# Performance work log

Measured on AMD Instinct MI355X. Metric: run time of the kernel, lower is better.

Reference implementation:

```python
import jax, jax.numpy as jnp
import numpy as np

N, E, D, H, O, G = 50000, 640000, 128, 128, 16, 64


def setup_inputs() -> dict:
    key = jax.random.key(0)
    ks = jax.random.split(key, 10)
    x = jax.random.normal(ks[0], (N, D), dtype=jnp.float32)
    edge_index = jax.random.randint(ks[1], (2, E), 0, N, dtype=jnp.int64)
    edge_weight = jax.random.uniform(ks[2], (E,), dtype=jnp.float32)
    batch = jnp.sort(jax.random.randint(ks[3], (N,), 0, G, dtype=jnp.int64))
    s1 = 1.0 / np.sqrt(D)
    s2 = 1.0 / np.sqrt(H)
    W1 = jax.random.uniform(ks[4], (D, H), jnp.float32, -s1, s1)
    b1 = jnp.zeros((H,), jnp.float32)
    W2 = jax.random.uniform(ks[5], (H, H), jnp.float32, -s2, s2)
    b2 = jnp.zeros((H,), jnp.float32)
    Wfc = jax.random.uniform(ks[6], (H, O), jnp.float32, -s2, s2)
    bfc = jax.random.uniform(ks[7], (O,), jnp.float32, -s2, s2)
    return dict(x=x, edge_index=edge_index, edge_weight=edge_weight, batch=batch,
                W1=W1, b1=b1, W2=W2, b2=b2, Wfc=Wfc, bfc=bfc)


def _gcn_conv(x, row, col, ew, W, b, n):
    # PyG GCNConv: out[i] = sum_{(j->i)} norm_ji * (x[j] @ W) + b
    xw = x @ W
    deg = jax.ops.segment_sum(ew, col, num_segments=n)          # [N]
    dinv = jnp.where(deg > 0, jax.lax.rsqrt(deg), 0.0)
    norm = dinv[row] * ew * dinv[col]                           # [E+N]
    msg = xw[row] * norm[:, None]                               # gather + scale
    return jax.ops.segment_sum(msg, col, num_segments=n) + b    # scatter-add


def reference(x, edge_index, edge_weight, batch, W1, b1, W2, b2, Wfc, bfc):
    n = x.shape[0]
    # add self-loops with weight 1 (PyG gcn_norm default)
    loop = jnp.arange(n, dtype=edge_index.dtype)
    row = jnp.concatenate([edge_index[0], loop])
    col = jnp.concatenate([edge_index[1], loop])
    ew = jnp.concatenate([edge_weight, jnp.ones((n,), edge_weight.dtype)])

    h = jax.nn.relu(_gcn_conv(x, row, col, ew, W1, b1, n))
    h = jax.nn.relu(_gcn_conv(h, row, col, ew, W2, b2, n))

    # global_mean_pool over graph ids
    sums = jax.ops.segment_sum(h, batch, num_segments=G)        # [G, H]
    cnt = jax.ops.segment_sum(jnp.ones((n,), h.dtype), batch, num_segments=G)
    pooled = sums / jnp.maximum(cnt, 1.0)[:, None]
    return pooled @ Wfc + bfc                                   # [G, O]
```

## Files before the change

### kernel.cpp

```cpp
#include <hip/hip_runtime.h>


typedef _Float16 h4 __attribute__((ext_vector_type(4)));
typedef _Float16 h8 __attribute__((ext_vector_type(8)));
typedef float f32x4 __attribute__((ext_vector_type(4)));

#define ELL 64

__global__ void build_pack_kernel(const int* __restrict__ row, const int* __restrict__ col,
                                  const float* __restrict__ ew, int* __restrict__ cnt,
                                  unsigned int* __restrict__ csr, int E, int NBe4,
                                  const float* __restrict__ W1, const float* __restrict__ W2,
                                  _Float16* __restrict__ Wp1, _Float16* __restrict__ Wp2) {
    if (blockIdx.x < (unsigned)NBe4) {
        int e0 = (blockIdx.x * 256 + threadIdx.x) * 4;
        if (e0 + 4 <= E) {
            int4 r4 = *(const int4*)(row + e0);
            int4 c4 = *(const int4*)(col + e0);
            float4 w4 = *(const float4*)(ew + e0);
            unsigned short hw0 = __builtin_bit_cast(unsigned short, (_Float16)w4.x);
            unsigned short hw1 = __builtin_bit_cast(unsigned short, (_Float16)w4.y);
            unsigned short hw2 = __builtin_bit_cast(unsigned short, (_Float16)w4.z);
            unsigned short hw3 = __builtin_bit_cast(unsigned short, (_Float16)w4.w);
            int s0 = atomicAdd(&cnt[c4.x], 1);
            int s1 = atomicAdd(&cnt[c4.y], 1);
            int s2 = atomicAdd(&cnt[c4.z], 1);
            int s3 = atomicAdd(&cnt[c4.w], 1);
            csr[(size_t)c4.x * ELL + s0] = ((unsigned int)r4.x << 16) | (unsigned int)hw0;
            csr[(size_t)c4.y * ELL + s1] = ((unsigned int)r4.y << 16) | (unsigned int)hw1;
            csr[(size_t)c4.z * ELL + s2] = ((unsigned int)r4.z << 16) | (unsigned int)hw2;
            csr[(size_t)c4.w * ELL + s3] = ((unsigned int)r4.w << 16) | (unsigned int)hw3;
        } else {
            for (int e = e0; e < E; ++e) {
                int c = col[e];
                int slot = atomicAdd(&cnt[c], 1);
                unsigned short hw = __builtin_bit_cast(unsigned short, (_Float16)ew[e]);
                csr[(size_t)c * ELL + slot] = ((unsigned int)row[e] << 16) | (unsigned int)hw;
            }
        }
        return;
    }
    int which = blockIdx.x - NBe4;
    const float* W = which ? W2 : W1;
    _Float16* Wp = which ? Wp2 : Wp1;
    for (int i = threadIdx.x; i < 2048; i += 256) {
        int lane = i & 63, kc = i >> 6;
        int c = kc >> 2, kb = kc & 3;
        int colq = lane & 15, quad = lane >> 4;
        h8 v;
#pragma unroll
        for (int j = 0; j < 8; ++j)
            v[j] = (_Float16)W[(kb * 32 + quad * 8 + j) * 128 + c * 16 + colq];
        ((h8*)Wp)[i] = v;
    }
}

__global__ __launch_bounds__(256) void deginv_convert_kernel(
        const float4* __restrict__ x4, const unsigned int* __restrict__ csr,
        const int* __restrict__ cnt, float* __restrict__ dinv,
        h4* __restrict__ p16, int n) {
    int node = blockIdx.x * 8 + (threadIdx.x >> 5);
    if (node >= n) return;
    int lane = threadIdx.x & 31;
    int cc = cnt[node];
    const unsigned int* base = csr + (size_t)node * ELL;
    float sum = 0.0f;
    for (int k = lane; k < cc; k += 32) {
        unsigned int v = __builtin_nontemporal_load(base + k);
        sum += (float)__builtin_bit_cast(_Float16, (unsigned short)(v & 0xffffu));
    }
#pragma unroll
    for (int m = 16; m >= 1; m >>= 1) sum += __shfl_xor(sum, m);
    float di = rsqrtf(1.0f + sum);
    if (lane == 0) dinv[node] = di;
    float4 v = x4[(size_t)node * 32 + lane];
    h4 h;
    h.x = (_Float16)(di * v.x); h.y = (_Float16)(di * v.y);
    h.z = (_Float16)(di * v.z); h.w = (_Float16)(di * v.w);
    p16[(size_t)node * 32 + lane] = h;
}

__global__ __launch_bounds__(256) void agg_kernel(const h4* __restrict__ in16,
                                                  const int* __restrict__ cnt,
                                                  const unsigned int* __restrict__ csr,
                                                  const float* __restrict__ dinv,
                                                  h4* __restrict__ out16, int n) {
    int node = blockIdx.x * 8 + (threadIdx.x >> 5);
    if (node >= n) return;
    int lane = threadIdx.x & 31;
    float di = dinv[node];
    h4 v = in16[(size_t)node * 32 + lane];
    float ax = (float)v.x, ay = (float)v.y, az = (float)v.z, aw = (float)v.w;
    int cc8 = (cnt[node] + 7) & ~7;
    const unsigned int* base = csr + (size_t)node * ELL;
    for (int idx = 0; idx < cc8; idx += 8) {
        unsigned int e[8];
        h4 u[8];
#pragma unroll
        for (int j = 0; j < 8; ++j) e[j] = __builtin_nontemporal_load(base + idx + j);
#pragma unroll
        for (int j = 0; j < 8; ++j) u[j] = in16[(size_t)(e[j] >> 16) * 32 + lane];
#pragma unroll
        for (int j = 0; j < 8; ++j) {
            float w = (float)__builtin_bit_cast(_Float16, (unsigned short)(e[j] & 0xffffu));
            ax += w * (float)u[j].x; ay += w * (float)u[j].y;
            az += w * (float)u[j].z; aw += w * (float)u[j].w;
        }
    }
    h4 r;
    r.x = (_Float16)(ax * di); r.y = (_Float16)(ay * di);
    r.z = (_Float16)(az * di); r.w = (_Float16)(aw * di);
    out16[(size_t)node * 32 + lane] = r;
}

template <int SCALE>
__global__ __launch_bounds__(256) void gemm_mfma(const _Float16* __restrict__ A,
                                                 const h8* __restrict__ Wp,
                                                 const float* __restrict__ bias,
                                                 const float* __restrict__ dinv,
                                                 _Float16* __restrict__ out16, int n) {
    int wid = threadIdx.x >> 6, lane = threadIdx.x & 63;
    int tb = blockIdx.x * 64 + wid * 16;
    if (tb >= n) return;
    int colq = lane & 15, quad = lane >> 4;

    int arow = tb + colq;
    if (arow >= n) arow = n - 1;
    const h8* Arow = (const h8*)(A + (size_t)arow * 128);
    h8 a[4];
#pragma unroll
    for (int kb = 0; kb < 4; ++kb) a[kb] = Arow[kb * 4 + quad];

    f32x4 acc[8];
#pragma unroll
    for (int c = 0; c < 8; ++c) acc[c] = (f32x4)(0.0f);

#pragma unroll
    for (int c = 0; c < 8; ++c) {
#pragma unroll
        for (int kb = 0; kb < 4; ++kb) {
            h8 b = Wp[(c * 4 + kb) * 64 + lane];
            acc[c] = __builtin_amdgcn_mfma_f32_16x16x32_f16(a[kb], b, acc[c], 0, 0, 0);
        }
    }

#pragma unroll
    for (int c = 0; c < 8; ++c) {
        float bz = bias[c * 16 + colq];
#pragma unroll
        for (int r = 0; r < 4; ++r) {
            int row = tb + quad * 4 + r;
            if (row < n) {
                float v = fmaxf(acc[c][r] + bz, 0.0f);
                if (SCALE) v *= dinv[row];
                out16[(size_t)row * 128 + c * 16 + colq] = (_Float16)v;
            }
        }
    }
}

__global__ __launch_bounds__(128) void pool_partial(const h4* __restrict__ h,
                                                    const int* __restrict__ batch,
                                                    float* __restrict__ pooled,
                                                    int n, int splits) {
    int g = blockIdx.x / splits;
    int s = blockIdx.x % splits;
    __shared__ int sb[2];
    __shared__ float4 red[128];
    int t = threadIdx.x;
    if (t < 2) {
        int target = g + t;
        int lo = 0, hi = n;
        while (lo < hi) { int m = (lo + hi) >> 1; if (batch[m] < target) lo = m + 1; else hi = m; }
        sb[t] = lo;
    }
    __syncthreads();
    int start = sb[0], end = sb[1], len = end - start;
    int a = start + (int)((long long)len * s / splits);
    int b = start + (int)((long long)len * (s + 1) / splits);
    int gq = t & 31;
    int seg = t >> 5;
    float4 acc; acc.x = acc.y = acc.z = acc.w = 0.0f;
    for (int i = a + seg; i < b; i += 4) {
        h4 v = h[(size_t)i * 32 + gq];
        acc.x += (float)v.x; acc.y += (float)v.y;
        acc.z += (float)v.z; acc.w += (float)v.w;
    }
    red[seg * 32 + gq] = acc;
    __syncthreads();
    if (t < 64) {
        float4 u = red[t], w = red[t + 64];
        u.x += w.x; u.y += w.y; u.z += w.z; u.w += w.w;
        red[t] = u;
    }
    __syncthreads();
    if (t < 32) {
        float4 u = red[t], w = red[t + 32];
        atomicAdd(&pooled[g * 128 + t * 4 + 0], u.x + w.x);
        atomicAdd(&pooled[g * 128 + t * 4 + 1], u.y + w.y);
        atomicAdd(&pooled[g * 128 + t * 4 + 2], u.z + w.z);
        atomicAdd(&pooled[g * 128 + t * 4 + 3], u.w + w.w);
    }
}

__global__ void fc_final(const float* __restrict__ pooled, const int* __restrict__ batch,
                         const float* __restrict__ Wfc, const float* __restrict__ bfc,
                         float* __restrict__ out, int n, int G, int O) {
    int gid = blockIdx.x * blockDim.x + threadIdx.x;
    if (gid >= G * O) return;
    int g = gid / O, o = gid % O;
    int lo = 0, hi = n;
    while (lo < hi) { int m = (lo + hi) >> 1; if (batch[m] < g) lo = m + 1; else hi = m; }
    int start = lo;
    lo = 0; hi = n;
    while (lo < hi) { int m = (lo + hi) >> 1; if (batch[m] < g + 1) lo = m + 1; else hi = m; }
    float inv = (lo > start) ? 1.0f / (float)(lo - start) : 0.0f;
    float a = bfc[o];
    for (int k = 0; k < 128; ++k) a += pooled[g * 128 + k] * inv * Wfc[k * O + o];
    out[gid] = a;
}

extern "C" void kernel_launch(void* const* d_in, const int* in_sizes, int n_in,
                              void* d_out, int out_size, void* d_ws, size_t ws_size,
                              hipStream_t stream) {
    const float* x     = (const float*)d_in[0];
    const int*   ei    = (const int*)d_in[1];
    const float* ew    = (const float*)d_in[2];
    const int*   batch = (const int*)d_in[3];
    const float* W1    = (const float*)d_in[4];
    const float* b1    = (const float*)d_in[5];
    const float* W2    = (const float*)d_in[6];
    const float* b2    = (const float*)d_in[7];
    const float* Wfc   = (const float*)d_in[8];
    const float* bfc   = (const float*)d_in[9];
    float* out = (float*)d_out;

    const int n = in_sizes[0] / 128;
    const int E = in_sizes[2];
    const int O = in_sizes[9];
    const int G = out_size / O;
    const int* row = ei;
    const int* col = ei + E;
    const int NBe4 = (E + 1023) / 1024;

    char* p = (char*)d_ws;
    auto alloc = [&](size_t bytes) {
        char* r = p;
        p += (bytes + 255) & ~(size_t)255;
        return r;
    };
    int*   cnt     = (int*)alloc((size_t)n * 4);
    float* pooled  = (float*)alloc((size_t)G * 128 * 4);
    unsigned int* csr = (unsigned int*)alloc((size_t)n * ELL * 4);
    char*  zend    = p;
    float* dinv    = (float*)alloc((size_t)n * 4);
    h4*    p1      = (h4*)alloc((size_t)n * 128 * 2);
    h4*    agg16   = (h4*)alloc((size_t)n * 128 * 2);
    h4*    p2      = (h4*)alloc((size_t)n * 128 * 2);
    h4*    h2      = (h4*)alloc((size_t)n * 128 * 2);
    _Float16* Wp1  = (_Float16*)alloc(128 * 128 * 2);
    _Float16* Wp2  = (_Float16*)alloc(128 * 128 * 2);

    hipMemsetAsync(cnt, 0, (size_t)(zend - (char*)cnt), stream);
    build_pack_kernel<<<NBe4 + 2, 256, 0, stream>>>(row, col, ew, cnt, csr, E, NBe4,
                                                    W1, W2, Wp1, Wp2);
    deginv_convert_kernel<<<(n + 7) / 8, 256, 0, stream>>>((const float4*)x, csr, cnt, dinv, p1, n);

    agg_kernel<<<(n + 7) / 8, 256, 0, stream>>>(p1, cnt, csr, dinv, agg16, n);
    gemm_mfma<1><<<(n + 63) / 64, 256, 0, stream>>>((const _Float16*)agg16, (const h8*)Wp1,
                                                    b1, dinv, (_Float16*)p2, n);

    agg_kernel<<<(n + 7) / 8, 256, 0, stream>>>(p2, cnt, csr, dinv, agg16, n);
    gemm_mfma<0><<<(n + 63) / 64, 256, 0, stream>>>((const _Float16*)agg16, (const h8*)Wp2,
                                                    b2, dinv, (_Float16*)h2, n);

    pool_partial<<<G * 8, 128, 0, stream>>>(h2, batch, pooled, n, 8);
    fc_final<<<(G * O + 255) / 256, 256, 0, stream>>>(pooled, batch, Wfc, bfc, out, n, G, O);
}
```

Before: 234.9 us.

## Fuse mean-pool partial sums into second GEMM epilogue and pad CSR rows

The second-layer GEMM now stages its ReLU output in shared memory and reduces rows into per-graph partial sums, issuing atomics into the pooled buffer directly. This removes the separate pooling kernel and the write and re-read of the final fp16 hidden matrix. The degree kernel also zero-pads each CSR row to a multiple of 8, which makes the memset of the large CSR region unnecessary, so it is dropped. The cost is extra shared memory and a serial per-column scan with atomics inside the GEMM blocks.

```diff
diff --git a/kernel.cpp b/kernel.cpp
--- a/kernel.cpp
+++ b/kernel.cpp
@@ -56,19 +56,21 @@
 }
 
 __global__ __launch_bounds__(256) void deginv_convert_kernel(
-        const float4* __restrict__ x4, const unsigned int* __restrict__ csr,
+        const float4* __restrict__ x4, unsigned int* __restrict__ csr,
         const int* __restrict__ cnt, float* __restrict__ dinv,
         h4* __restrict__ p16, int n) {
     int node = blockIdx.x * 8 + (threadIdx.x >> 5);
     if (node >= n) return;
     int lane = threadIdx.x & 31;
     int cc = cnt[node];
-    const unsigned int* base = csr + (size_t)node * ELL;
+    unsigned int* base = csr + (size_t)node * ELL;
     float sum = 0.0f;
     for (int k = lane; k < cc; k += 32) {
-        unsigned int v = __builtin_nontemporal_load(base + k);
+        unsigned int v = base[k];
         sum += (float)__builtin_bit_cast(_Float16, (unsigned short)(v & 0xffffu));
     }
+    int cc8 = (cc + 7) & ~7;
+    if (lane < cc8 - cc) base[cc + lane] = 0u;
 #pragma unroll
     for (int m = 16; m >= 1; m >>= 1) sum += __shfl_xor(sum, m);
     float di = rsqrtf(1.0f + sum);
@@ -113,93 +115,78 @@
     out16[(size_t)node * 32 + lane] = r;
 }
 
-template <int SCALE>
+template <int POOL>
 __global__ __launch_bounds__(256) void gemm_mfma(const _Float16* __restrict__ A,
                                                  const h8* __restrict__ Wp,
                                                  const float* __restrict__ bias,
                                                  const float* __restrict__ dinv,
-                                                 _Float16* __restrict__ out16, int n) {
+                                                 _Float16* __restrict__ out16,
+                                                 const int* __restrict__ batch,
+                                                 float* __restrict__ pooled, int n) {
+    __shared__ float ls[POOL ? 64 * 132 : 1];
     int wid = threadIdx.x >> 6, lane = threadIdx.x & 63;
-    int tb = blockIdx.x * 64 + wid * 16;
-    if (tb >= n) return;
+    int tbb = blockIdx.x * 64;
+    int tb = tbb + wid * 16;
     int colq = lane & 15, quad = lane >> 4;
 
-    int arow = tb + colq;
-    if (arow >= n) arow = n - 1;
-    const h8* Arow = (const h8*)(A + (size_t)arow * 128);
-    h8 a[4];
-#pragma unroll
-    for (int kb = 0; kb < 4; ++kb) a[kb] = Arow[kb * 4 + quad];
-
-    f32x4 acc[8];
-#pragma unroll
-    for (int c = 0; c < 8; ++c) acc[c] = (f32x4)(0.0f);
-
-#pragma unroll
-    for (int c = 0; c < 8; ++c) {
-#pragma unroll
-        for (int kb = 0; kb < 4; ++kb) {
-            h8 b = Wp[(c * 4 + kb) * 64 + lane];
-            acc[c] = __builtin_amdgcn_mfma_f32_16x16x32_f16(a[kb], b, acc[c], 0, 0, 0);
-        }
-    }
-
-#pragma unroll
-    for (int c = 0; c < 8; ++c) {
-        float bz = bias[c * 16 + colq];
-#pragma unroll
-        for (int r = 0; r < 4; ++r) {
-            int row = tb + quad * 4 + r;
-            if (row < n) {
-                float v = fmaxf(acc[c][r] + bz, 0.0f);
-                if (SCALE) v *= dinv[row];
-                out16[(size_t)row * 128 + c * 16 + colq] = (_Float16)v;
-            }
-        }
-    }
-}
-
-__global__ __launch_bounds__(128) void pool_partial(const h4* __restrict__ h,
-                                                    const int* __restrict__ batch,
-                                                    float* __restrict__ pooled,
-                                                    int n, int splits) {
-    int g = blockIdx.x / splits;
-    int s = blockIdx.x % splits;
-    __shared__ int sb[2];
-    __shared__ float4 red[128];
-    int t = threadIdx.x;
-    if (t < 2) {
-        int target = g + t;
-        int lo = 0, hi = n;
-        while (lo < hi) { int m = (lo + hi) >> 1; if (batch[m] < target) lo = m + 1; else hi = m; }
-        sb[t] = lo;
-    }
-    __syncthreads();
-    int start = sb[0], end = sb[1], len = end - start;
-    int a = start + (int)((long long)len * s / splits);
-    int b = start + (int)((long long)len * (s + 1) / splits);
-    int gq = t & 31;
-    int seg = t >> 5;
-    float4 acc; acc.x = acc.y = acc.z = acc.w = 0.0f;
-    for (int i = a + seg; i < b; i += 4) {
-        h4 v = h[(size_t)i * 32 + gq];
-        acc.x += (float)v.x; acc.y += (float)v.y;
-        acc.z += (float)v.z; acc.w += (float)v.w;
-    }
-    red[seg * 32 + gq] = acc;
-    __syncthreads();
-    if (t < 64) {
-        float4 u = red[t], w = red[t + 64];
-        u.x += w.x; u.y += w.y; u.z += w.z; u.w += w.w;
-        red[t] = u;
-    }
-    __syncthreads();
-    if (t < 32) {
-        float4 u = red[t], w = red[t + 32];
-        atomicAdd(&pooled[g * 128 + t * 4 + 0], u.x + w.x);
-        atomicAdd(&pooled[g * 128 + t * 4 + 1], u.y + w.y);
-        atomicAdd(&pooled[g * 128 + t * 4 + 2], u.z + w.z);
-        atomicAdd(&pooled[g * 128 + t * 4 + 3], u.w + w.w);
+    if (tb < n) {
+        int arow = tb + colq;
+        if (arow >= n) arow = n - 1;
+        const h8* Arow = (const h8*)(A + (size_t)arow * 128);
+        h8 a[4];
+#pragma unroll
+        for (int kb = 0; kb < 4; ++kb) a[kb] = Arow[kb * 4 + quad];
+
+        f32x4 acc[8];
+#pragma unroll
+        for (int c = 0; c < 8; ++c) acc[c] = (f32x4)(0.0f);
+
+#pragma unroll
+        for (int c = 0; c < 8; ++c) {
+#pragma unroll
+            for (int kb = 0; kb < 4; ++kb) {
+                h8 b = Wp[(c * 4 + kb) * 64 + lane];
+                acc[c] = __builtin_amdgcn_mfma_f32_16x16x32_f16(a[kb], b, acc[c], 0, 0, 0);
+            }
+        }
+
+#pragma unroll
+        for (int c = 0; c < 8; ++c) {
+            float bz = bias[c * 16 + colq];
+#pragma unroll
+            for (int r = 0; r < 4; ++r) {
+                int rl = wid * 16 + quad * 4 + r;
+                int row = tbb + rl;
+                if (row < n) {
+                    float v = fmaxf(acc[c][r] + bz, 0.0f);
+                    if (POOL) {
+                        ls[rl * 132 + c * 16 + colq] = v;
+                    } else {
+                        out16[(size_t)row * 128 + c * 16 + colq] = (_Float16)(v * dinv[row]);
+                    }
+                }
+            }
+        }
+    }
+
+    if (POOL) {
+        __syncthreads();
+        int colp = threadIdx.x & 127;
+        int half = threadIdx.x >> 7;
+        int r0 = half * 32, r1 = r0 + 32;
+        float accp = 0.0f;
+        int cur = -1;
+        for (int rl = r0; rl < r1; ++rl) {
+            int gr = tbb + rl;
+            if (gr >= n) break;
+            int g = batch[gr];
+            if (g != cur) {
+                if (cur >= 0) atomicAdd(&pooled[cur * 128 + colp], accp);
+                cur = g; accp = 0.0f;
+            }
+            accp += ls[rl * 132 + colp];
+        }
+        if (cur >= 0) atomicAdd(&pooled[cur * 128 + colp], accp);
     }
 }
 
@@ -251,13 +238,12 @@
     };
     int*   cnt     = (int*)alloc((size_t)n * 4);
     float* pooled  = (float*)alloc((size_t)G * 128 * 4);
+    char*  zend    = p;
     unsigned int* csr = (unsigned int*)alloc((size_t)n * ELL * 4);
-    char*  zend    = p;
     float* dinv    = (float*)alloc((size_t)n * 4);
     h4*    p1      = (h4*)alloc((size_t)n * 128 * 2);
     h4*    agg16   = (h4*)alloc((size_t)n * 128 * 2);
     h4*    p2      = (h4*)alloc((size_t)n * 128 * 2);
-    h4*    h2      = (h4*)alloc((size_t)n * 128 * 2);
     _Float16* Wp1  = (_Float16*)alloc(128 * 128 * 2);
     _Float16* Wp2  = (_Float16*)alloc(128 * 128 * 2);
 
@@ -267,13 +253,12 @@
     deginv_convert_kernel<<<(n + 7) / 8, 256, 0, stream>>>((const float4*)x, csr, cnt, dinv, p1, n);
 
     agg_kernel<<<(n + 7) / 8, 256, 0, stream>>>(p1, cnt, csr, dinv, agg16, n);
-    gemm_mfma<1><<<(n + 63) / 64, 256, 0, stream>>>((const _Float16*)agg16, (const h8*)Wp1,
-                                                    b1, dinv, (_Float16*)p2, n);
+    gemm_mfma<0><<<(n + 63) / 64, 256, 0, stream>>>((const _Float16*)agg16, (const h8*)Wp1,
+                                                    b1, dinv, (_Float16*)p2, batch, pooled, n);
 
     agg_kernel<<<(n + 7) / 8, 256, 0, stream>>>(p2, cnt, csr, dinv, agg16, n);
-    gemm_mfma<0><<<(n + 63) / 64, 256, 0, stream>>>((const _Float16*)agg16, (const h8*)Wp2,
-                                                    b2, dinv, (_Float16*)h2, n);
-
-    pool_partial<<<G * 8, 128, 0, stream>>>(h2, batch, pooled, n, 8);
+    gemm_mfma<1><<<(n + 63) / 64, 256, 0, stream>>>((const _Float16*)agg16, (const h8*)Wp2,
+                                                    b2, dinv, nullptr, batch, pooled, n);
+
     fc_final<<<(G * O + 255) / 256, 256, 0, stream>>>(pooled, batch, Wfc, bfc, out, n, G, O);
 }
```

Result: faster. 223.9 us (median of 2 runs) (-4.7%).
